# Kernel optimization log

Hardware: AMD Instinct MI355X
Metric: run time of the kernel (lower is better)

Reference implementation:

```python
import jax, jax.numpy as jnp
import numpy as np


def mha_col0(x0, w_in, b_in, w_out, b_out):
    # x0: [N, D]. torch MHA (1 head, batch_first=False): seq dim = N, this is the
    # batch-0 slice (the only one consumed by tmp[:, 0]).
    qkv = x0 @ w_in.T + b_in                     # [N, 3D]
    q, k, v = jnp.split(qkv, 3, axis=-1)         # each [N, D]
    scale = 1.0 / np.sqrt(np.float32(q.shape[-1]))
    attn = jax.nn.softmax((q * scale) @ k.T, axis=-1)   # [N, N]
    return (attn @ v) @ w_out.T + b_out          # [N, D]


def sage(x_src, x_dst, ei, w_l, b_l, w_r):
    # PyG SAGEConv with aggr='sum': out = lin_l(sum_j x_src[src_j]) + lin_r(x_dst)
    msg = x_src[ei[0]]                                            # [E, D] gather
    agg = jax.ops.segment_sum(msg, ei[1], num_segments=x_dst.shape[0])  # [Nd, D] scatter
    return agg @ w_l.T + b_l + x_dst @ w_r.T


def setup_inputs() -> dict:
    key = jax.random.key(0)
    ks = jax.random.split(key, 24)
    N, C, D, E = 8192, 6, 128, 262144
    s = 0.05
    p = lambda k, shape: jax.random.normal(k, shape, dtype=jnp.float32) * s
    return {
        "x_A": jax.random.normal(ks[0], (N, C, D), dtype=jnp.float32),
        "x_B": jax.random.normal(ks[1], (N, C, D), dtype=jnp.float32),
        "ei_AB": jax.random.randint(ks[2], (2, E), 0, N),
        "ei_BA": jax.random.randint(ks[3], (2, E), 0, N),
        "ei_AA": jax.random.randint(ks[4], (2, E), 0, N),
        "inW_A": p(ks[5], (3 * D, D)), "inB_A": p(ks[6], (3 * D,)),
        "outW_A": p(ks[7], (D, D)), "outB_A": p(ks[8], (D,)),
        "inW_B": p(ks[9], (3 * D, D)), "inB_B": p(ks[10], (3 * D,)),
        "outW_B": p(ks[11], (D, D)), "outB_B": p(ks[12], (D,)),
        "wl_AB": p(ks[13], (D, D)), "bl_AB": p(ks[14], (D,)), "wr_AB": p(ks[15], (D, D)),
        "wl_BA": p(ks[16], (D, D)), "bl_BA": p(ks[17], (D,)), "wr_BA": p(ks[18], (D, D)),
        "wl_AA": p(ks[19], (D, D)), "bl_AA": p(ks[20], (D,)), "wr_AA": p(ks[21], (D, D)),
    }


def reference(x_A, x_B, ei_AB, ei_BA, ei_AA,
              inW_A, inB_A, outW_A, outB_A,
              inW_B, inB_B, outW_B, outB_B,
              wl_AB, bl_AB, wr_AB,
              wl_BA, bl_BA, wr_BA,
              wl_AA, bl_AA, wr_AA):
    # per-type attention, keeping only column 0 (tmp[:, 0])
    h_A = mha_col0(x_A[:, 0], inW_A, inB_A, outW_A, outB_A)   # [N, D]
    h_B = mha_col0(x_B[:, 0], inW_B, inB_B, outW_B, outB_B)   # [N, D]
    # HeteroConv(aggr='sum'): B gets A->B; A gets B->A + A->A
    out_B = sage(h_A, h_B, ei_AB, wl_AB, bl_AB, wr_AB)
    out_A = (sage(h_B, h_A, ei_BA, wl_BA, bl_BA, wr_BA)
             + sage(h_A, h_A, ei_AA, wl_AA, bl_AA, wr_AA))
    # re-attach remaining column tokens (x is 3D)
    new_A = jnp.concatenate((out_A[:, None, :], x_A[:, 1:]), axis=1)  # [N, C, D]
    new_B = jnp.concatenate((out_B[:, None, :], x_B[:, 1:]), axis=1)
    return new_A, new_B
```

## Files before the change

kernel.cpp:

```cpp
#include <hip/hip_runtime.h>
#include <hip/hip_bf16.h>

typedef unsigned short u16;
typedef unsigned int u32;
typedef __attribute__((ext_vector_type(8))) short bf16x8;
typedef __attribute__((ext_vector_type(4))) short bf16x4;
typedef __attribute__((ext_vector_type(4))) float f32x4;
typedef __attribute__((ext_vector_type(16))) float f32x16;

#define MFMA(a,b,c)   __builtin_amdgcn_mfma_f32_16x16x32_bf16((a),(b),(c),0,0,0)
#define MFMA32(a,b,c) __builtin_amdgcn_mfma_f32_32x32x16_bf16((a),(b),(c),0,0,0)

__device__ __forceinline__ float bf2f(u16 u){
  union { float f; u32 i; } c; c.i = ((u32)u) << 16; return c.f;
}
__device__ __forceinline__ u16 f2bf(float f){
  __hip_bfloat16 h = __float2bfloat16(f);
  u16 u; __builtin_memcpy(&u, &h, 2); return u;
}
__device__ __forceinline__ bf16x8 ld8f(const float* p){
  bf16x8 r;
  #pragma unroll
  for (int i = 0; i < 8; i++) r[i] = (short)f2bf(p[i]);
  return r;
}
__device__ __forceinline__ u32 cvtpk(float a, float b){
  u32 r; asm volatile("v_cvt_pk_bf16_f32 %0, %1, %2" : "=v"(r) : "v"(a), "v"(b)); return r;
}
__device__ __forceinline__ void pl32swap(u32 &a, u32 &b){
  asm volatile("v_permlane32_swap_b32 %0, %1" : "+v"(a), "+v"(b));
}

#define QSCALE 0.12751741528681559f

struct WPrepArgs { const float* src[10]; int off[10]; int total4; };
__global__ __launch_bounds__(256) void prelude_kernel(
    WPrepArgs a, u16* __restrict__ wdst,
    const int* __restrict__ e0, const int* __restrict__ e1, const int* __restrict__ e2,
    int* __restrict__ cnt,
    const float* __restrict__ xA, float* __restrict__ outA,
    const float* __restrict__ xB, float* __restrict__ outB,
    int Nn, int E, int W, int HB, int TB)
{
  const int tid = threadIdx.x;
  int b = blockIdx.x;
  if (b < W) {
    int i = b * 256 + tid;
    if (i >= a.total4) return;
    int e = i * 4;
    int j = 0;
    #pragma unroll
    for (int k = 1; k < 10; k++) if (e >= a.off[k]) j = k;
    f32x4 v = *(const f32x4*)(a.src[j] + (e - a.off[j]));
    bf16x4 o;
    #pragma unroll
    for (int r = 0; r < 4; r++) o[r] = (short)f2bf(v[r]);
    *(bf16x4*)(wdst + e) = o;
    return;
  }
  b -= W;
  if (b < 3 * HB) {
    int t = b / HB;
    int e = (b % HB) * 256 + tid;
    if (e >= E) return;
    const int* ei = t == 0 ? e0 : (t == 1 ? e1 : e2);
    atomicAdd(&cnt[t * Nn + ei[E + e]], 1);
    return;
  }
  b -= 3 * HB;
  {
    int t = b / TB;
    int idx = (b % TB) * 256 + tid;
    if (idx >= Nn * 160) return;
    const float* x = t ? xB : xA;
    float* o = t ? outB : outA;
    int n = idx / 160, r = idx % 160;
    size_t off = (size_t)n * 768 + 128 + (size_t)r * 4;
    *(f32x4*)(o + off) = *(const f32x4*)(x + off);
  }
}

__global__ __launch_bounds__(256) void qkv_scan_kernel(
    const float* __restrict__ xA, const u16* __restrict__ wA, const float* __restrict__ bA, u16* __restrict__ yA,
    const float* __restrict__ xB, const u16* __restrict__ wB, const float* __restrict__ bB, u16* __restrict__ yB,
    u16* __restrict__ vtA_, u16* __restrict__ vtB_,
    const int* __restrict__ cnt, int* __restrict__ off, int* __restrict__ work,
    int Nn, int N, int LB)
{
  const int tid = threadIdx.x;
  int b = blockIdx.x;
  if (b >= 2 * LB) {
    const int t = b - 2 * LB;
    const int* c = cnt + t * Nn;
    int* o = off + t * (Nn + 1);
    int* w = work + t * Nn;
    __shared__ int part[256];
    const int base = tid * 32;
    int loc[32], s = 0;
    #pragma unroll
    for (int i = 0; i < 32; i++) { loc[i] = s; s += c[base + i]; }
    part[tid] = s;
    __syncthreads();
    #pragma unroll
    for (int st = 1; st < 256; st <<= 1) {
      int v = (tid >= st) ? part[tid - st] : 0;
      __syncthreads();
      part[tid] += v;
      __syncthreads();
    }
    int pre = (tid == 0) ? 0 : part[tid - 1];
    #pragma unroll
    for (int i = 0; i < 32; i++) { int p = pre + loc[i]; o[base + i] = p; w[base + i] = p; }
    if (tid == 255) o[Nn] = part[255];
    return;
  }
  const int yb = b & 1, xb = b >> 1;
  const float* x = yb ? xB : xA;
  const u16* w = yb ? wB : wA;
  const float* bb = yb ? bB : bA;
  u16* y = yb ? yB : yA;
  u16* vt = yb ? vtB_ : vtA_;
  const int lane = tid & 63, wid = tid >> 6;
  const int g = lane >> 4, l15 = lane & 15;
  const int row0 = xb * 64 + wid * 16;

  bf16x8 a[4];
  const float* xr = x + (size_t)(row0 + l15) * 768;
  #pragma unroll
  for (int kk = 0; kk < 4; kk++) a[kk] = ld8f(xr + kk * 32 + g * 8);

  const f32x4 fz = {0.f, 0.f, 0.f, 0.f};
  for (int j0 = 0; j0 < 384; j0 += 16) {
    f32x4 acc = fz;
    const u16* wr_ = w + (size_t)(j0 + l15) * 128;
    #pragma unroll
    for (int kk = 0; kk < 4; kk++)
      acc = MFMA(a[kk], *(const bf16x8*)(wr_ + kk * 32 + g * 8), acc);
    float bv = bb[j0 + l15];
    if (j0 < 128) {
      #pragma unroll
      for (int r = 0; r < 4; r++)
        y[(size_t)(row0 + g * 4 + r) * 256 + j0 + l15] = f2bf((acc[r] + bv) * QSCALE);
    } else if (j0 < 256) {
      #pragma unroll
      for (int r = 0; r < 4; r++)
        y[(size_t)(row0 + g * 4 + r) * 256 + j0 + l15] = f2bf(acc[r] + bv);
    } else {
      bf16x4 o4;
      #pragma unroll
      for (int r = 0; r < 4; r++) o4[r] = (short)f2bf(acc[r] + bv);
      *(bf16x4*)(vt + (size_t)(j0 - 256 + l15) * N + row0 + g * 4) = o4;
    }
  }
}

__global__ __launch_bounds__(256, 3) void flash_sort_kernel(
    const u16* __restrict__ qkvA, const u16* __restrict__ vtA,
    const u16* __restrict__ qkvB, const u16* __restrict__ vtB,
    u16* __restrict__ part_acc, float* __restrict__ part_l,
    const int* __restrict__ e0, const int* __restrict__ e1, const int* __restrict__ e2,
    int* __restrict__ work, int* __restrict__ ssrc,
    int N, int segsz, int SEG, int NB128, int FB, int HB, int E)
{
  __shared__ __align__(16) u16 Kt[2][32 * 128];
  __shared__ __align__(16) u16 Vtt[2][64 * 64];
  const int tid = threadIdx.x;
  int b = blockIdx.x;
  if (b >= FB) {
    int sb = b - FB;
    int t = sb / HB;
    int e = (sb % HB) * 256 + tid;
    if (e >= E) return;
    const int* ei = t == 0 ? e0 : (t == 1 ? e1 : e2);
    int s = ei[e], d = ei[E + e];
    int pos = atomicAdd(&work[t * N + d], 1);
    ssrc[(size_t)t * E + pos] = s;
    return;
  }
  const int x = b % NB128;
  const int rest = b / NB128;
  const int seg = rest % SEG;
  const int ty = rest / SEG;
  const u16* qkv = ty ? qkvB : qkvA;
  const u16* vt  = ty ? vtB  : vtA;
  const int lane = tid & 63, wid = tid >> 6;
  const int l31 = lane & 31, h = lane >> 5, l7 = lane & 7;
  const int q = x * 128 + wid * 32 + l31;
  const int kvbase = seg * segsz;

  int rk[2], ck[2], cks[2], vd[2], vc[2], vidx[2];
  #pragma unroll
  for (int i = 0; i < 2; i++) {
    int ch = tid + i * 256;
    rk[i] = ch >> 4; ck[i] = (ch & 15) * 8; cks[i] = ck[i] ^ ((rk[i] & 7) << 3);
    int d = ch >> 2, c8 = (ch & 3) * 8;
    vd[i] = d; vc[i] = c8;
    int row = d & 63, col = (c8 + ((d >> 6) << 5)) ^ ((row & 7) << 3);
    vidx[i] = row * 64 + col;
  }

  bf16x8 aQ[8];
  const u16* qr = qkv + (size_t)q * 256;
  #pragma unroll
  for (int kk = 0; kk < 8; kk++) aQ[kk] = *(const bf16x8*)(qr + kk * 16 + h * 8);

  f32x16 accO[4];
  #pragma unroll
  for (int d = 0; d < 4; d++) accO[d] = (f32x16)0.f;
  float l_ = 0.f;

  {
    #pragma unroll
    for (int i = 0; i < 2; i++) {
      bf16x8 kv8 = *(const bf16x8*)(qkv + 128 + (size_t)(kvbase + rk[i]) * 256 + ck[i]);
      bf16x8 vv8 = *(const bf16x8*)(vt + (size_t)vd[i] * N + kvbase + vc[i]);
      *(bf16x8*)&Kt[0][rk[i] * 128 + cks[i]] = kv8;
      *(bf16x8*)&Vtt[0][vidx[i]] = vv8;
    }
  }
  __syncthreads();

  int cur = 0;
  for (int kt = 0; kt < segsz; kt += 32) {
    const bool pfch = (kt + 32 < segsz);
    bf16x8 kreg[2], vreg[2];
    if (pfch) {
      const int kv0n = kvbase + kt + 32;
      #pragma unroll
      for (int i = 0; i < 2; i++) {
        kreg[i] = *(const bf16x8*)(qkv + 128 + (size_t)(kv0n + rk[i]) * 256 + ck[i]);
        vreg[i] = *(const bf16x8*)(vt + (size_t)vd[i] * N + kv0n + vc[i]);
      }
    }

    const u16* KtC = Kt[cur];
    const u16* VtC = Vtt[cur];

    f32x16 sc = (f32x16)0.f;
    #pragma unroll
    for (int kk = 0; kk < 8; kk++) {
      bf16x8 aK = *(bf16x8*)&KtC[l31 * 128 + (((kk * 2 + h) * 8) ^ (l7 << 3))];
      sc = MFMA32(aK, aQ[kk], sc);
    }

    #pragma unroll
    for (int i = 0; i < 16; i++) {
      float e = __builtin_exp2f(sc[i]);
      sc[i] = e; l_ += e;
    }

    #pragma unroll
    for (int t = 0; t < 2; t++) {
      const int jA = t * 2, jB = t * 2 + 1;
      u32 a0 = cvtpk(sc[jA * 4 + 0], sc[jA * 4 + 1]);
      u32 b0 = cvtpk(sc[jB * 4 + 0], sc[jB * 4 + 1]);
      u32 a1 = cvtpk(sc[jA * 4 + 2], sc[jA * 4 + 3]);
      u32 b1 = cvtpk(sc[jB * 4 + 2], sc[jB * 4 + 3]);
      pl32swap(a0, b0); pl32swap(a1, b1);
      union { u32 w[4]; bf16x8 v; } pf;
      pf.w[0] = a0; pf.w[1] = a1; pf.w[2] = b0; pf.w[3] = b1;
      #pragma unroll
      for (int db = 0; db < 4; db++) {
        const int row = (db & 1) * 32 + l31;
        const int col = (t * 16 + h * 8 + ((db >> 1) << 5)) ^ (l7 << 3);
        bf16x8 aV = *(bf16x8*)&VtC[row * 64 + col];
        accO[db] = MFMA32(aV, pf.v, accO[db]);
      }
    }

    if (pfch) {
      const int nb = cur ^ 1;
      #pragma unroll
      for (int i = 0; i < 2; i++) {
        *(bf16x8*)&Kt[nb][rk[i] * 128 + cks[i]] = kreg[i];
        *(bf16x8*)&Vtt[nb][vidx[i]] = vreg[i];
      }
    }
    __syncthreads();
    cur ^= 1;
  }

  l_ += __shfl_xor(l_, 32);

  const size_t pbase = ((size_t)(ty * SEG + seg) * N + q) * 128;
  #pragma unroll
  for (int d = 0; d < 4; d++)
    #pragma unroll
    for (int j = 0; j < 4; j++) {
      bf16x4 o4;
      #pragma unroll
      for (int r = 0; r < 4; r++) o4[r] = (short)f2bf(accO[d][j * 4 + r]);
      *(bf16x4*)(part_acc + pbase + d * 32 + j * 8 + h * 4) = o4;
    }
  if (h == 0)
    part_l[(size_t)(ty * SEG + seg) * N + q] = l_;
}

__global__ __launch_bounds__(256) void combine_hproj_kernel(
    const u16* __restrict__ part_acc, const float* __restrict__ part_l,
    const u16* __restrict__ woutA, const float* __restrict__ boutA, u16* __restrict__ hA,
    const u16* __restrict__ woutB, const float* __restrict__ boutB, u16* __restrict__ hB,
    int N, int SEG)
{
  __shared__ __align__(16) u16 ot[64 * 136];
  const int t = blockIdx.y;
  const u16* w = t ? woutB : woutA;
  const float* bb = t ? boutB : boutA;
  u16* hOut = t ? hB : hA;
  const int tid = threadIdx.x;
  const int row = tid >> 2, qt = tid & 3;
  const int grow = blockIdx.x * 64 + row;

  float l = 0.f;
  for (int s = 0; s < SEG; s++)
    l += part_l[(size_t)(t * SEG + s) * N + grow];
  float acc[32];
  #pragma unroll
  for (int i = 0; i < 32; i++) acc[i] = 0.f;
  for (int s = 0; s < SEG; s++) {
    const u16* pa = part_acc + ((size_t)(t * SEG + s) * N + grow) * 128 + qt * 32;
    #pragma unroll
    for (int j = 0; j < 4; j++) {
      bf16x8 vch = *(const bf16x8*)(pa + j * 8);
      #pragma unroll
      for (int i = 0; i < 8; i++) acc[j * 8 + i] += bf2f((u16)vch[i]);
    }
  }
  const float inv = 1.f / l;
  #pragma unroll
  for (int j = 0; j < 4; j++) {
    bf16x8 oc;
    #pragma unroll
    for (int i = 0; i < 8; i++) oc[i] = (short)f2bf(acc[j * 8 + i] * inv);
    *(bf16x8*)&ot[row * 136 + qt * 32 + j * 8] = oc;
  }
  __syncthreads();

  const int lane = tid & 63, wid = tid >> 6;
  const int g = lane >> 4, l15 = lane & 15;
  const int row0 = wid * 16;
  bf16x8 a[4];
  #pragma unroll
  for (int kk = 0; kk < 4; kk++) a[kk] = *(bf16x8*)&ot[(row0 + l15) * 136 + kk * 32 + g * 8];
  const f32x4 fz = {0.f, 0.f, 0.f, 0.f};
  for (int j0 = 0; j0 < 128; j0 += 16) {
    f32x4 acc2 = fz;
    const u16* wr_ = w + (size_t)(j0 + l15) * 128;
    #pragma unroll
    for (int kk = 0; kk < 4; kk++)
      acc2 = MFMA(a[kk], *(const bf16x8*)(wr_ + kk * 32 + g * 8), acc2);
    float bv = bb[j0 + l15];
    #pragma unroll
    for (int r = 0; r < 4; r++)
      hOut[(size_t)(blockIdx.x * 64 + row0 + g * 4 + r) * 128 + j0 + l15] = f2bf(acc2[r] + bv);
  }
}

__global__ __launch_bounds__(256) void aggregate_kernel(
    const u16* __restrict__ h0, const u16* __restrict__ h1, const u16* __restrict__ h2,
    const int* __restrict__ off, const int* __restrict__ ssrc,
    u16* __restrict__ agg, int Nn, int E)
{
  const int t = blockIdx.y;
  const u16* h = t == 0 ? h0 : (t == 1 ? h1 : h2);
  const int* o = off + t * (Nn + 1);
  const int* ss = ssrc + (size_t)t * E;
  u16* a = agg + (size_t)t * Nn * 128;
  const int wid = threadIdx.x >> 6, lane = threadIdx.x & 63;
  const int d = blockIdx.x * 4 + wid;
  const int s0 = o[d], s1 = o[d + 1];
  float a0 = 0.f, a1 = 0.f;
  int e = s0;
  for (; e + 3 < s1; e += 4) {
    int r0 = ss[e], r1 = ss[e + 1], r2 = ss[e + 2], r3 = ss[e + 3];
    u32 v0 = *(const u32*)(h + (size_t)r0 * 128 + lane * 2);
    u32 v1 = *(const u32*)(h + (size_t)r1 * 128 + lane * 2);
    u32 v2 = *(const u32*)(h + (size_t)r2 * 128 + lane * 2);
    u32 v3 = *(const u32*)(h + (size_t)r3 * 128 + lane * 2);
    a0 += bf2f((u16)(v0 & 0xffff)) + bf2f((u16)(v1 & 0xffff)) + bf2f((u16)(v2 & 0xffff)) + bf2f((u16)(v3 & 0xffff));
    a1 += bf2f((u16)(v0 >> 16)) + bf2f((u16)(v1 >> 16)) + bf2f((u16)(v2 >> 16)) + bf2f((u16)(v3 >> 16));
  }
  for (; e < s1; e++) {
    u32 v = *(const u32*)(h + (size_t)ss[e] * 128 + lane * 2);
    a0 += bf2f((u16)(v & 0xffff));
    a1 += bf2f((u16)(v >> 16));
  }
  *(u32*)(a + (size_t)d * 128 + lane * 2) = cvtpk(a0, a1);
}

__global__ __launch_bounds__(256) void sage_out_kernel(
    const u16* __restrict__ aggAB, const u16* __restrict__ wlAB, const float* __restrict__ blAB,
    const u16* __restrict__ hB, const u16* __restrict__ wrAB,
    const u16* __restrict__ aggBA, const u16* __restrict__ wlBA, const float* __restrict__ blBA,
    const u16* __restrict__ hA, const u16* __restrict__ wrBA,
    const u16* __restrict__ aggAA, const u16* __restrict__ wlAA, const float* __restrict__ blAA,
    const u16* __restrict__ wrAA,
    float* __restrict__ outA, float* __restrict__ outB)
{
  const bool two = (blockIdx.y == 1);
  const u16* agg1 = two ? aggBA : aggAB;
  const u16* wl1  = two ? wlBA  : wlAB;
  const float* bl1 = two ? blBA : blAB;
  const u16* h1   = two ? hA : hB;
  const u16* wr1  = two ? wrBA : wrAB;
  float* out = two ? outA : outB;

  const int lane = threadIdx.x & 63, wid = threadIdx.x >> 6;
  const int g = lane >> 4, l15 = lane & 15;
  const int row0 = blockIdx.x * 64 + wid * 16;

  bf16x8 a1[4], aH1[4], a2[4];
  const u16* ar1 = agg1 + (size_t)(row0 + l15) * 128;
  const u16* hr1 = h1 + (size_t)(row0 + l15) * 128;
  #pragma unroll
  for (int kk = 0; kk < 4; kk++) {
    a1[kk] = *(const bf16x8*)(ar1 + kk * 32 + g * 8);
    aH1[kk] = *(const bf16x8*)(hr1 + kk * 32 + g * 8);
  }
  if (two) {
    const u16* ar2 = aggAA + (size_t)(row0 + l15) * 128;
    #pragma unroll
    for (int kk = 0; kk < 4; kk++)
      a2[kk] = *(const bf16x8*)(ar2 + kk * 32 + g * 8);
  }

  const f32x4 fz = {0.f, 0.f, 0.f, 0.f};
  for (int j0 = 0; j0 < 128; j0 += 16) {
    f32x4 acc = fz;
    const u16* w1 = wl1 + (size_t)(j0 + l15) * 128;
    const u16* w2 = wr1 + (size_t)(j0 + l15) * 128;
    #pragma unroll
    for (int kk = 0; kk < 4; kk++) {
      acc = MFMA(a1[kk], *(const bf16x8*)(w1 + kk * 32 + g * 8), acc);
      acc = MFMA(aH1[kk], *(const bf16x8*)(w2 + kk * 32 + g * 8), acc);
    }
    float bias = bl1[j0 + l15];
    if (two) {
      const u16* w3 = wlAA + (size_t)(j0 + l15) * 128;
      const u16* w4 = wrAA + (size_t)(j0 + l15) * 128;
      #pragma unroll
      for (int kk = 0; kk < 4; kk++) {
        acc = MFMA(a2[kk], *(const bf16x8*)(w3 + kk * 32 + g * 8), acc);
        acc = MFMA(aH1[kk], *(const bf16x8*)(w4 + kk * 32 + g * 8), acc);
      }
      bias += blAA[j0 + l15];
    }
    #pragma unroll
    for (int r = 0; r < 4; r++)
      out[(size_t)(row0 + g * 4 + r) * 768 + j0 + l15] = acc[r] + bias;
  }
}

extern "C" void kernel_launch(void* const* d_in, const int* in_sizes, int n_in,
                              void* d_out, int out_size, void* d_ws, size_t ws_size,
                              hipStream_t stream)
{
  const int D = 128, C = 6;
  const int N = in_sizes[0] / (C * D);
  const int E = in_sizes[2] / 2;

  const float* xA = (const float*)d_in[0];
  const float* xB = (const float*)d_in[1];
  const int* eiAB = (const int*)d_in[2];
  const int* eiBA = (const int*)d_in[3];
  const int* eiAA = (const int*)d_in[4];
  const float* inW_A  = (const float*)d_in[5];
  const float* inB_A  = (const float*)d_in[6];
  const float* outW_A = (const float*)d_in[7];
  const float* outB_A = (const float*)d_in[8];
  const float* inW_B  = (const float*)d_in[9];
  const float* inB_B  = (const float*)d_in[10];
  const float* outW_B = (const float*)d_in[11];
  const float* outB_B = (const float*)d_in[12];
  const float* wlAB = (const float*)d_in[13];
  const float* blAB = (const float*)d_in[14];
  const float* wrAB = (const float*)d_in[15];
  const float* wlBA = (const float*)d_in[16];
  const float* blBA = (const float*)d_in[17];
  const float* wrBA = (const float*)d_in[18];
  const float* wlAA = (const float*)d_in[19];
  const float* blAA = (const float*)d_in[20];
  const float* wrAA = (const float*)d_in[21];

  u16* qkvA = (u16*)d_ws;
  u16* qkvB = qkvA + (size_t)N * 256;
  u16* vtA  = qkvB + (size_t)N * 256;
  u16* vtB  = vtA + (size_t)D * N;
  u16* hA   = vtB + (size_t)D * N;
  u16* hB   = hA + (size_t)N * D;
  u16* wbf  = hB + (size_t)N * D;
  const int wsz[10] = {3*D*D, 3*D*D, D*D, D*D, D*D, D*D, D*D, D*D, D*D, D*D};
  const float* wsrc[10] = {inW_A, inW_B, outW_A, outW_B, wlAB, wrAB, wlBA, wrBA, wlAA, wrAA};
  WPrepArgs wp; int wtot = 0;
  for (int k = 0; k < 10; k++) { wp.src[k] = wsrc[k]; wp.off[k] = wtot; wtot += wsz[k]; }
  wp.total4 = wtot / 4;
  u16* w_inA  = wbf + wp.off[0];
  u16* w_inB  = wbf + wp.off[1];
  u16* w_outA = wbf + wp.off[2];
  u16* w_outB = wbf + wp.off[3];
  u16* w_wlAB = wbf + wp.off[4];
  u16* w_wrAB = wbf + wp.off[5];
  u16* w_wlBA = wbf + wp.off[6];
  u16* w_wrBA = wbf + wp.off[7];
  u16* w_wlAA = wbf + wp.off[8];
  u16* w_wrAA = wbf + wp.off[9];

  int* cnt  = (int*)(wbf + wtot);
  int* off  = cnt + 3 * N;
  int* work = off + 3 * (N + 1);
  int* ssrc = work + 3 * N;
  char* uni = (char*)(ssrc + 3 * E);
  size_t base_b = (size_t)(uni - (char*)d_ws);
  size_t agg_b = (size_t)3 * N * 128 * 2;
  auto part_b = [&](int S){ return (size_t)2 * S * N * 128 * 2 + (size_t)2 * S * N * 4; };
  int SEG = 8;
  while (SEG > 1 && ws_size < base_b + (part_b(SEG) > agg_b ? part_b(SEG) : agg_b)) SEG >>= 1;
  const int segsz = N / SEG;
  u16* part_acc = (u16*)uni;
  float* part_l = (float*)(part_acc + (size_t)2 * SEG * N * 128);
  u16* aggAB = (u16*)uni;
  u16* aggBA = aggAB + (size_t)N * D;
  u16* aggAA = aggBA + (size_t)N * D;

  float* outA = (float*)d_out;
  float* outB = outA + (size_t)N * C * D;

  dim3 blk(256);
  const int W = (wp.total4 + 255) / 256;
  const int HB = (E + 255) / 256;
  const int TB = (N * 160 + 255) / 256;
  const int LB = N / 64;
  const int NB128 = N / 128;
  const int FB = NB128 * SEG * 2;
  (void)hipMemsetAsync(cnt, 0, (size_t)3 * N * sizeof(int), stream);
  prelude_kernel<<<dim3(W + 3 * HB + 2 * TB), blk, 0, stream>>>(
      wp, wbf, eiAB, eiBA, eiAA, cnt, xA, outA, xB, outB, N, E, W, HB, TB);
  qkv_scan_kernel<<<dim3(2 * LB + 3), blk, 0, stream>>>(
      xA, w_inA, inB_A, qkvA, xB, w_inB, inB_B, qkvB, vtA, vtB,
      cnt, off, work, N, N, LB);
  flash_sort_kernel<<<dim3(FB + 3 * HB), blk, 0, stream>>>(
      qkvA, vtA, qkvB, vtB, part_acc, part_l,
      eiAB, eiBA, eiAA, work, ssrc, N, segsz, SEG, NB128, FB, HB, E);
  combine_hproj_kernel<<<dim3(N / 64, 2), blk, 0, stream>>>(part_acc, part_l,
                                                            w_outA, outB_A, hA,
                                                            w_outB, outB_B, hB, N, SEG);
  aggregate_kernel<<<dim3(N / 4, 3), blk, 0, stream>>>(hA, hB, hA, off, ssrc, aggAB, N, E);
  sage_out_kernel<<<dim3(N / 64, 2), blk, 0, stream>>>(
      aggAB, w_wlAB, blAB, hB, w_wrAB,
      aggBA, w_wlBA, blBA, hA, w_wrBA,
      aggAA, w_wlAA, blAA, w_wrAA, outA, outB);
}
```

Before: 246.6 us.

## Use per-wave direct global-to-LDS loads in flash attention, drop block barriers

```diff
diff --git a/kernel.cpp b/kernel.cpp
--- a/kernel.cpp
+++ b/kernel.cpp
@@ -29,6 +29,10 @@
 }
 __device__ __forceinline__ void pl32swap(u32 &a, u32 &b){
   asm volatile("v_permlane32_swap_b32 %0, %1" : "+v"(a), "+v"(b));
+}
+__device__ __forceinline__ void gll16(const void* g, void* l){
+  __builtin_amdgcn_global_load_lds((const __attribute__((address_space(1))) void*)g,
+                                   (__attribute__((address_space(3))) void*)l, 16, 0, 0);
 }
 
 #define QSCALE 0.12751741528681559f
@@ -154,7 +158,7 @@
   }
 }
 
-__global__ __launch_bounds__(256, 3) void flash_sort_kernel(
+__global__ __launch_bounds__(256, 2) void flash_sort_kernel(
     const u16* __restrict__ qkvA, const u16* __restrict__ vtA,
     const u16* __restrict__ qkvB, const u16* __restrict__ vtB,
     u16* __restrict__ part_acc, float* __restrict__ part_l,
@@ -162,8 +166,7 @@
     int* __restrict__ work, int* __restrict__ ssrc,
     int N, int segsz, int SEG, int NB128, int FB, int HB, int E)
 {
-  __shared__ __align__(16) u16 Kt[2][32 * 128];
-  __shared__ __align__(16) u16 Vtt[2][64 * 64];
+  __shared__ __align__(16) u16 KV[4][8192];
   const int tid = threadIdx.x;
   int b = blockIdx.x;
   if (b >= FB) {
@@ -177,10 +180,11 @@
     ssrc[(size_t)t * E + pos] = s;
     return;
   }
-  const int x = b % NB128;
-  const int rest = b / NB128;
-  const int seg = rest % SEG;
-  const int ty = rest / SEG;
+  const int NG = 2 * SEG;
+  const int grp = b % NG;
+  const int x = b / NG;
+  const int seg = grp % SEG;
+  const int ty = grp / SEG;
   const u16* qkv = ty ? qkvB : qkvA;
   const u16* vt  = ty ? vtB  : vtA;
   const int lane = tid & 63, wid = tid >> 6;
@@ -188,16 +192,25 @@
   const int q = x * 128 + wid * 32 + l31;
   const int kvbase = seg * segsz;
 
-  int rk[2], ck[2], cks[2], vd[2], vc[2], vidx[2];
-  #pragma unroll
-  for (int i = 0; i < 2; i++) {
-    int ch = tid + i * 256;
-    rk[i] = ch >> 4; ck[i] = (ch & 15) * 8; cks[i] = ck[i] ^ ((rk[i] & 7) << 3);
-    int d = ch >> 2, c8 = (ch & 3) * 8;
-    vd[i] = d; vc[i] = c8;
-    int row = d & 63, col = (c8 + ((d >> 6) << 5)) ^ ((row & 7) << 3);
-    vidx[i] = row * 64 + col;
-  }
+  u16* Kw = &KV[wid][0];
+  u16* Vw = &KV[wid][4096];
+
+  u32 koff[8], voff[8];
+  #pragma unroll
+  for (int i = 0; i < 8; i++) {
+    int r = i * 4 + (lane >> 4);
+    int cs = (lane & 15) ^ (r & 7);
+    koff[i] = (u32)(r * 512 + 256 + cs * 16);
+  }
+  #pragma unroll
+  for (int j = 0; j < 8; j++) {
+    int lr = j * 8 + (lane >> 3);
+    int ch = (lane & 7) ^ (lr & 7);
+    int d  = lr + ((ch >> 2) << 6);
+    voff[j] = (u32)d * (u32)(N * 2) + (u32)((ch & 3) * 16);
+  }
+  const char* qkvb = (const char*)qkv;
+  const char* vtb  = (const char*)vt;
 
   bf16x8 aQ[8];
   const u16* qr = qkv + (size_t)q * 256;
@@ -209,38 +222,30 @@
   for (int d = 0; d < 4; d++) accO[d] = (f32x16)0.f;
   float l_ = 0.f;
 
-  {
-    #pragma unroll
-    for (int i = 0; i < 2; i++) {
-      bf16x8 kv8 = *(const bf16x8*)(qkv + 128 + (size_t)(kvbase + rk[i]) * 256 + ck[i]);
-      bf16x8 vv8 = *(const bf16x8*)(vt + (size_t)vd[i] * N + kvbase + vc[i]);
-      *(bf16x8*)&Kt[0][rk[i] * 128 + cks[i]] = kv8;
-      *(bf16x8*)&Vtt[0][vidx[i]] = vv8;
-    }
-  }
-  __syncthreads();
-
-  int cur = 0;
-  for (int kt = 0; kt < segsz; kt += 32) {
-    const bool pfch = (kt + 32 < segsz);
-    bf16x8 kreg[2], vreg[2];
-    if (pfch) {
-      const int kv0n = kvbase + kt + 32;
-      #pragma unroll
-      for (int i = 0; i < 2; i++) {
-        kreg[i] = *(const bf16x8*)(qkv + 128 + (size_t)(kv0n + rk[i]) * 256 + ck[i]);
-        vreg[i] = *(const bf16x8*)(vt + (size_t)vd[i] * N + kv0n + vc[i]);
-      }
-    }
-
-    const u16* KtC = Kt[cur];
-    const u16* VtC = Vtt[cur];
+  size_t kb = (size_t)kvbase * 512;
+  size_t vb = (size_t)kvbase * 2;
+  #pragma unroll
+  for (int i = 0; i < 8; i++) gll16(qkvb + kb + koff[i], (char*)Kw + i * 1024);
+  #pragma unroll
+  for (int j = 0; j < 8; j++) gll16(vtb + vb + voff[j], (char*)Vw + j * 1024);
+
+  const int nt = segsz >> 5;
+  for (int t = 0; t < nt; t++) {
+    const bool more = (t + 1 < nt);
+    asm volatile("s_waitcnt vmcnt(8)" ::: "memory");
+    __builtin_amdgcn_sched_barrier(0);
 
     f32x16 sc = (f32x16)0.f;
     #pragma unroll
     for (int kk = 0; kk < 8; kk++) {
-      bf16x8 aK = *(bf16x8*)&KtC[l31 * 128 + (((kk * 2 + h) * 8) ^ (l7 << 3))];
+      bf16x8 aK = *(bf16x8*)&Kw[l31 * 128 + (((kk * 2 + h) * 8) ^ (l7 << 3))];
       sc = MFMA32(aK, aQ[kk], sc);
+    }
+
+    if (more) {
+      __builtin_amdgcn_sched_barrier(0);
+      #pragma unroll
+      for (int i = 0; i < 8; i++) gll16(qkvb + kb + 16384 + koff[i], (char*)Kw + i * 1024);
     }
 
     #pragma unroll
@@ -249,9 +254,13 @@
       sc[i] = e; l_ += e;
     }
 
-    #pragma unroll
-    for (int t = 0; t < 2; t++) {
-      const int jA = t * 2, jB = t * 2 + 1;
+    if (more) asm volatile("s_waitcnt vmcnt(8)" ::: "memory");
+    else      asm volatile("s_waitcnt vmcnt(0)" ::: "memory");
+    __builtin_amdgcn_sched_barrier(0);
+
+    #pragma unroll
+    for (int t2 = 0; t2 < 2; t2++) {
+      const int jA = t2 * 2, jB = t2 * 2 + 1;
       u32 a0 = cvtpk(sc[jA * 4 + 0], sc[jA * 4 + 1]);
       u32 b0 = cvtpk(sc[jB * 4 + 0], sc[jB * 4 + 1]);
       u32 a1 = cvtpk(sc[jA * 4 + 2], sc[jA * 4 + 3]);
@@ -262,22 +271,18 @@
       #pragma unroll
       for (int db = 0; db < 4; db++) {
         const int row = (db & 1) * 32 + l31;
-        const int col = (t * 16 + h * 8 + ((db >> 1) << 5)) ^ (l7 << 3);
-        bf16x8 aV = *(bf16x8*)&VtC[row * 64 + col];
+        const int col = (t2 * 16 + h * 8 + ((db >> 1) << 5)) ^ (l7 << 3);
+        bf16x8 aV = *(bf16x8*)&Vw[row * 64 + col];
         accO[db] = MFMA32(aV, pf.v, accO[db]);
       }
     }
 
-    if (pfch) {
-      const int nb = cur ^ 1;
-      #pragma unroll
-      for (int i = 0; i < 2; i++) {
-        *(bf16x8*)&Kt[nb][rk[i] * 128 + cks[i]] = kreg[i];
-        *(bf16x8*)&Vtt[nb][vidx[i]] = vreg[i];
-      }
-    }
-    __syncthreads();
-    cur ^= 1;
+    if (more) {
+      __builtin_amdgcn_sched_barrier(0);
+      #pragma unroll
+      for (int j = 0; j < 8; j++) gll16(vtb + vb + 64 + voff[j], (char*)Vw + j * 1024);
+      kb += 16384; vb += 64;
+    }
   }
 
   l_ += __shfl_xor(l_, 32);
@@ -513,7 +518,7 @@
   size_t base_b = (size_t)(uni - (char*)d_ws);
   size_t agg_b = (size_t)3 * N * 128 * 2;
   auto part_b = [&](int S){ return (size_t)2 * S * N * 128 * 2 + (size_t)2 * S * N * 4; };
-  int SEG = 8;
+  int SEG = 4;
   while (SEG > 1 && ws_size < base_b + (part_b(SEG) > agg_b ? part_b(SEG) : agg_b)) SEG >>= 1;
   const int segsz = N / SEG;
   u16* part_acc = (u16*)uni;
```

Result: no change. 246.9 us (+0.1%).
